# Performance work log

Measured on AMD Instinct MI355X. Metric: run time of the kernel, lower is better.

## Reference

```python
import jax, jax.numpy as jnp
import numpy as np

EMBED_DIM = 128
HIDDEN = 64
LN_EPS = 1e-5
NORM_EPS = 1e-6


def setup_inputs() -> dict:
    key = jax.random.key(0)
    ks = jax.random.split(key, 12)
    B, L = 32, 2048
    inp = {
        "map_lane_positions": jax.random.normal(ks[0], (B, L, 10, 2), dtype=jnp.float32),
        "map_is_intersection": jax.random.randint(ks[1], (B, L), 0, 3, dtype=jnp.int64),
        "map_turn_direction": jax.random.randint(ks[2], (B, L), 0, 3, dtype=jnp.int64),
        "map_traffic_control": jax.random.randint(ks[3], (B, L), 0, 2, dtype=jnp.int64),
        # SingleInputEmbedding params: Linear(2,64) -> LayerNorm(64) -> ReLU -> Linear(64,128)
        "W1": jax.random.normal(ks[4], (2, HIDDEN), dtype=jnp.float32) * 0.5,
        "b1": jax.random.normal(ks[5], (HIDDEN,), dtype=jnp.float32) * 0.1,
        "ln_gamma": jnp.ones((HIDDEN,), dtype=jnp.float32),
        "ln_beta": jnp.zeros((HIDDEN,), dtype=jnp.float32),
        "W2": jax.random.normal(ks[6], (HIDDEN, EMBED_DIM), dtype=jnp.float32) * 0.1,
        "b2": jax.random.normal(ks[7], (EMBED_DIM,), dtype=jnp.float32) * 0.1,
        # discrete embedding tables
        "E_intersection": jax.random.normal(ks[8], (3, EMBED_DIM), dtype=jnp.float32),
        "E_turn": jax.random.normal(ks[9], (3, EMBED_DIM), dtype=jnp.float32),
        "E_traffic": jax.random.normal(ks[10], (2, EMBED_DIM), dtype=jnp.float32),
    }
    return inp


def _mlp(x, W1, b1, g, beta, W2, b2):
    h = x @ W1 + b1                                  # [..., 64]
    mu = jnp.mean(h, axis=-1, keepdims=True)
    var = jnp.mean((h - mu) ** 2, axis=-1, keepdims=True)
    h = (h - mu) * jax.lax.rsqrt(var + LN_EPS) * g + beta
    h = jax.nn.relu(h)
    return h @ W2 + b2                               # [..., 128]


def reference(map_lane_positions, map_is_intersection, map_turn_direction,
              map_traffic_control, W1, b1, ln_gamma, ln_beta, W2, b2,
              E_intersection, E_turn, E_traffic):
    # direction vectors between consecutive points: [B, L, 9, 2]
    dv = map_lane_positions[:, :, 1:, :] - map_lane_positions[:, :, :-1, :]
    norms = jnp.sqrt(jnp.sum(dv ** 2, axis=-1, keepdims=True) + NORM_EPS)
    dv = dv / norms

    cont = _mlp(dv, W1, b1, ln_gamma, ln_beta, W2, b2)   # [B, L, 9, 128]
    # discrete embeddings broadcast over the 9-point axis
    disc = (E_intersection[map_is_intersection]
            + E_turn[map_turn_direction]
            + E_traffic[map_traffic_control])             # [B, L, 128]
    fused = cont + disc[:, :, None, :]                    # [B, L, 9, 128]
    return jnp.max(fused, axis=2)                         # [B, L, 128]
```

## Files before the change

kernel.cpp:

```cpp
#include <hip/hip_runtime.h>
#include <hip/hip_bf16.h>

#define NB      16
#define THREADS 256

#define WS_CST4   0
#define WS_QUAD   256
#define WS_DISC   272
#define WS_W2     2576

typedef float f32x4  __attribute__((ext_vector_type(4)));
typedef short bf16x8 __attribute__((ext_vector_type(8)));

static __device__ __forceinline__ unsigned f2bf(float f) {
    __hip_bfloat16 h = __float2bfloat16(f);
    return (unsigned)__builtin_bit_cast(unsigned short, h);
}

__global__ __launch_bounds__(THREADS)
void lane_setup_kernel(const float* __restrict__ W1, const float* __restrict__ b1,
                       const float* __restrict__ gam, const float* __restrict__ bet,
                       const float* __restrict__ W2, const float* __restrict__ b2,
                       const float* __restrict__ Ei, const float* __restrict__ Et,
                       const float* __restrict__ Etc, float* __restrict__ ws)
{
    const int tid = threadIdx.x, lane = tid & 63, wv = tid >> 6;

    if (wv == 0) {
        float wx = W1[lane], wy = W1[64 + lane], bb = b1[lane];
        float sx = wx, sy = wy, sb = bb;
        #pragma unroll
        for (int m = 1; m < 64; m <<= 1) {
            sx += __shfl_xor(sx, m, 64);
            sy += __shfl_xor(sy, m, 64);
            sb += __shfl_xor(sb, m, 64);
        }
        float a = wx - sx * (1.f / 64.f);
        float b = wy - sy * (1.f / 64.f);
        float c = bb - sb * (1.f / 64.f);
        float p0 = a * a, p1 = b * b, p2 = a * b, p3 = a * c, p4 = b * c, p5 = c * c;
        #pragma unroll
        for (int m = 1; m < 64; m <<= 1) {
            p0 += __shfl_xor(p0, m, 64); p1 += __shfl_xor(p1, m, 64);
            p2 += __shfl_xor(p2, m, 64); p3 += __shfl_xor(p3, m, 64);
            p4 += __shfl_xor(p4, m, 64); p5 += __shfl_xor(p5, m, 64);
        }
        float g = gam[lane];
        ((float4*)(ws + WS_CST4))[lane] = make_float4(a * g, b * g, c * g, bet[lane]);
        if (lane == 0) {
            ws[WS_QUAD + 0] = p0 * (1.f / 64.f);
            ws[WS_QUAD + 1] = p1 * (1.f / 64.f);
            ws[WS_QUAD + 2] = p2 * (1.f / 64.f);
            ws[WS_QUAD + 3] = p3 * (1.f / 64.f);
            ws[WS_QUAD + 4] = p4 * (1.f / 64.f);
            ws[WS_QUAD + 5] = p5 * (1.f / 64.f) + 1e-5f;
        }
    }

    {
        uint4* dst = (uint4*)(ws + WS_W2);
        #pragma unroll
        for (int f = wv * 4; f < wv * 4 + 4; ++f) {
            int c = f >> 1, kt = f & 1;
            int col = c * 16 + (lane & 15);
            int k0  = kt * 32 + (lane >> 4) * 8;
            unsigned w[4];
            #pragma unroll
            for (int j = 0; j < 4; ++j) {
                unsigned lo = f2bf(W2[(k0 + 2 * j) * 128 + col]);
                unsigned hi = f2bf(W2[(k0 + 2 * j + 1) * 128 + col]);
                w[j] = (hi << 16) | lo;
            }
            dst[f * 64 + lane] = make_uint4(w[0], w[1], w[2], w[3]);
        }
    }

    for (int i = tid; i < 18 * 128; i += THREADS) {
        int combo = i >> 7, col = i & 127;
        int ai = combo / 6; int r = combo - ai * 6; int bi = r >> 1; int ci = r & 1;
        ws[WS_DISC + i] = b2[col] + Ei[ai * 128 + col] + Et[bi * 128 + col] + Etc[ci * 128 + col];
    }
}

__global__ __launch_bounds__(THREADS)
void lane_node_embed_mfma(const float* __restrict__ pos,
                          const int*   __restrict__ idx_int,
                          const int*   __restrict__ idx_turn,
                          const int*   __restrict__ idx_tc,
                          const float* __restrict__ ws,
                          float* __restrict__ out,
                          int n_nodes)
{
    __shared__ unsigned short H[NB * 9 * 64];
    __shared__ float4 smv[NB * 9];
    __shared__ int    cmb_lds[NB];

    const int tid  = threadIdx.x;
    const int lane = tid & 63;
    const int wv   = __builtin_amdgcn_readfirstlane(tid >> 6);
    const int blockStart = blockIdx.x * NB;

    const float4 cst = ((const float4*)(ws + WS_CST4))[lane];

    const int ct0 = wv * 2;
    const uint4* wfr = (const uint4*)(ws + WS_W2);
    bf16x8 Bfr[2][2];
    #pragma unroll
    for (int c = 0; c < 2; ++c)
        #pragma unroll
        for (int kt = 0; kt < 2; ++kt)
            Bfr[c][kt] = __builtin_bit_cast(bf16x8, wfr[((ct0 + c) * 2 + kt) * 64 + lane]);

    if (tid < NB * 9) {
        int nd = tid / 9, p = tid - nd * 9;
        int gn = blockStart + nd;
        float ax = 0.f, ay = 0.f, is = 0.f;
        if (gn < n_nodes) {
            const float2* pp = (const float2*)pos + (size_t)gn * 10 + p;
            float2 q0 = pp[0], q1 = pp[1];
            float dx = q1.x - q0.x, dy = q1.y - q0.y;
            float inv = rsqrtf(fmaf(dx, dx, fmaf(dy, dy, 1e-6f)));
            dx *= inv; dy *= inv;
            float qA = ws[WS_QUAD + 0], qB = ws[WS_QUAD + 1], qC = ws[WS_QUAD + 2];
            float qD = ws[WS_QUAD + 3], qE = ws[WS_QUAD + 4], qF = ws[WS_QUAD + 5];
            float t   = fmaf(dx * dy, qC, fmaf(dx, qD, dy * qE));
            float var = fmaf(2.f, t, fmaf(dx * dx, qA, fmaf(dy * dy, qB, qF)));
            is = rsqrtf(var);
            ax = dx * is; ay = dy * is;
        }
        smv[tid] = make_float4(ax, ay, is, 0.f);
    }
    if (tid < NB) {
        int gn = blockStart + tid;
        cmb_lds[tid] = (gn < n_nodes)
            ? (idx_int[gn] * 3 + idx_turn[gn]) * 2 + idx_tc[gn] : 0;
    }
    __syncthreads();

    {
        const int klo    = lane & 7;
        const int kchunk = lane >> 3;
        #pragma unroll
        for (int i = 0; i < 4; ++i) {
            int node = wv * 4 + i;
            int s = node & 7;
            int widx = node * 576 + ((kchunk ^ s) << 3) + klo;
            #pragma unroll
            for (int p = 0; p < 9; ++p) {
                float4 t = smv[node * 9 + p];
                float h = fmaf(t.x, cst.x, fmaf(t.y, cst.y, fmaf(t.z, cst.z, cst.w)));
                h = fmaxf(h, 0.f);
                H[widx + p * 64] = (unsigned short)f2bf(h);
            }
        }
    }
    __syncthreads();

    const int g   = lane >> 4;
    const int l15 = lane & 15;
    const int sr  = l15 & 7;
    const int idx0 = l15 * 576 + (((0 + g) ^ sr) << 3);
    const int idx1 = l15 * 576 + (((4 + g) ^ sr) << 3);

    f32x4 mx0 = {-INFINITY, -INFINITY, -INFINITY, -INFINITY};
    f32x4 mx1 = mx0;
    const f32x4 zz = {0.f, 0.f, 0.f, 0.f};
    #pragma unroll
    for (int p = 0; p < 9; ++p) {
        bf16x8 a0 = *(const bf16x8*)&H[idx0 + p * 64];
        bf16x8 a1 = *(const bf16x8*)&H[idx1 + p * 64];
        f32x4 t0 = __builtin_amdgcn_mfma_f32_16x16x32_bf16(a0, Bfr[0][0], zz, 0, 0, 0);
        t0       = __builtin_amdgcn_mfma_f32_16x16x32_bf16(a1, Bfr[0][1], t0, 0, 0, 0);
        f32x4 t1 = __builtin_amdgcn_mfma_f32_16x16x32_bf16(a0, Bfr[1][0], zz, 0, 0, 0);
        t1       = __builtin_amdgcn_mfma_f32_16x16x32_bf16(a1, Bfr[1][1], t1, 0, 0, 0);
        #pragma unroll
        for (int k = 0; k < 4; ++k) {
            mx0[k] = fmaxf(mx0[k], t0[k]);
            mx1[k] = fmaxf(mx1[k], t1[k]);
        }
    }

    #pragma unroll
    for (int c = 0; c < 2; ++c) {
        int col = (ct0 + c) * 16 + l15;
        f32x4 m = (c == 0) ? mx0 : mx1;
        #pragma unroll
        for (int j = 0; j < 4; ++j) {
            int nd = g * 4 + j;
            int gn = blockStart + nd;
            if (gn < n_nodes) {
                float dv = ws[WS_DISC + cmb_lds[nd] * 128 + col];
                out[(size_t)gn * 128 + col] = m[j] + dv;
            }
        }
    }
}

extern "C" void kernel_launch(void* const* d_in, const int* in_sizes, int n_in,
                              void* d_out, int out_size, void* d_ws, size_t ws_size,
                              hipStream_t stream) {
    const float* pos  = (const float*)d_in[0];
    const int*   ii   = (const int*)  d_in[1];
    const int*   it   = (const int*)  d_in[2];
    const int*   itc  = (const int*)  d_in[3];
    const float* W1   = (const float*)d_in[4];
    const float* b1   = (const float*)d_in[5];
    const float* gam  = (const float*)d_in[6];
    const float* bet  = (const float*)d_in[7];
    const float* W2   = (const float*)d_in[8];
    const float* b2   = (const float*)d_in[9];
    const float* Ei   = (const float*)d_in[10];
    const float* Et   = (const float*)d_in[11];
    const float* Etc  = (const float*)d_in[12];
    float* out = (float*)d_out;
    float* ws  = (float*)d_ws;

    int n_nodes = in_sizes[1];
    int blocks  = (n_nodes + NB - 1) / NB;

    hipLaunchKernelGGL(lane_setup_kernel, dim3(1), dim3(THREADS), 0, stream,
                       W1, b1, gam, bet, W2, b2, Ei, Et, Etc, ws);
    hipLaunchKernelGGL(lane_node_embed_mfma, dim3(blocks), dim3(THREADS), 0, stream,
                       pos, ii, it, itc, ws, out, n_nodes);
}
```

Baseline: 34.83 us.

## Process four node tiles per block with double-buffered LDS and prefetched positions

Each block now handles four 16-node tiles in sequence, loading the W2 fragments and LN constants once per block instead of once per 16 nodes. Hidden activations live in a double-buffered LDS array, and the next tile's position loads are issued before the current tile's MFMA phase, so global latency overlaps compute. The small-vector stash is made wave-local with an lgkmcnt wait instead of a block barrier. The inverse std is stored implicitly and recovered with a sqrt. Each lane now packs two bf16 hidden values per LDS write, and discrete-index lookups are spread across lanes with shuffles. The cost is four times fewer blocks, which lowers parallelism, plus a small numeric difference from recomputing the scale.

```diff
diff --git a/kernel.cpp b/kernel.cpp
--- a/kernel.cpp
+++ b/kernel.cpp
@@ -2,6 +2,7 @@
 #include <hip/hip_bf16.h>
 
 #define NB      16
+#define TILES   4
 #define THREADS 256
 
 #define WS_CST4   0
@@ -91,16 +92,20 @@
                           float* __restrict__ out,
                           int n_nodes)
 {
-    __shared__ unsigned short H[NB * 9 * 64];
-    __shared__ float4 smv[NB * 9];
-    __shared__ int    cmb_lds[NB];
+    __shared__ __align__(16) unsigned short H[2][NB * 9 * 64];
+    __shared__ float2 smv[NB * 9];
 
     const int tid  = threadIdx.x;
     const int lane = tid & 63;
     const int wv   = __builtin_amdgcn_readfirstlane(tid >> 6);
-    const int blockStart = blockIdx.x * NB;
-
-    const float4 cst = ((const float4*)(ws + WS_CST4))[lane];
+    const int blockBase = blockIdx.x * (NB * TILES);
+
+    const float qA = ws[WS_QUAD + 0], qB = ws[WS_QUAD + 1], qC = ws[WS_QUAD + 2];
+    const float qD = ws[WS_QUAD + 3], qE = ws[WS_QUAD + 4], qF = ws[WS_QUAD + 5];
+
+    const int kl = lane & 31;
+    const float4 cstA = ((const float4*)(ws + WS_CST4))[2 * kl];
+    const float4 cstB = ((const float4*)(ws + WS_CST4))[2 * kl + 1];
 
     const int ct0 = wv * 2;
     const uint4* wfr = (const uint4*)(ws + WS_W2);
@@ -111,88 +116,109 @@
         for (int kt = 0; kt < 2; ++kt)
             Bfr[c][kt] = __builtin_bit_cast(bf16x8, wfr[((ct0 + c) * 2 + kt) * 64 + lane]);
 
-    if (tid < NB * 9) {
-        int nd = tid / 9, p = tid - nd * 9;
-        int gn = blockStart + nd;
-        float ax = 0.f, ay = 0.f, is = 0.f;
-        if (gn < n_nodes) {
-            const float2* pp = (const float2*)pos + (size_t)gn * 10 + p;
-            float2 q0 = pp[0], q1 = pp[1];
+    const int sn = lane / 9;
+    const int sp = lane - sn * 9;
+    const int sNodeT = wv * 4 + sn;
+    const bool sAct = (lane < 36);
+
+    float2 q0 = make_float2(0.f, 0.f), q1 = q0;
+
+    const int half = lane >> 5;
+    const int kch  = kl >> 2;
+    const int kofs = (2 * kl) & 7;
+
+    const int l15 = lane & 15, g = lane >> 4;
+    const int sr  = l15 & 7;
+    const int i0  = l15 * 576 + ((g ^ sr) << 3);
+    const int i1  = l15 * 576 + (((4 + g) ^ sr) << 3);
+
+    auto issuePos = [&](int t) {
+        if (sAct) {
+            int gn = blockBase + t * NB + sNodeT;
+            if (gn < n_nodes) {
+                const float2* pp = (const float2*)pos + (size_t)gn * 10 + sp;
+                q0 = pp[0]; q1 = pp[1];
+            } else { q0 = make_float2(0.f, 0.f); q1 = q0; }
+        }
+    };
+
+    auto stashA = [&](int buf) {
+        if (sAct) {
             float dx = q1.x - q0.x, dy = q1.y - q0.y;
             float inv = rsqrtf(fmaf(dx, dx, fmaf(dy, dy, 1e-6f)));
             dx *= inv; dy *= inv;
-            float qA = ws[WS_QUAD + 0], qB = ws[WS_QUAD + 1], qC = ws[WS_QUAD + 2];
-            float qD = ws[WS_QUAD + 3], qE = ws[WS_QUAD + 4], qF = ws[WS_QUAD + 5];
-            float t   = fmaf(dx * dy, qC, fmaf(dx, qD, dy * qE));
-            float var = fmaf(2.f, t, fmaf(dx * dx, qA, fmaf(dy * dy, qB, qF)));
-            is = rsqrtf(var);
-            ax = dx * is; ay = dy * is;
-        }
-        smv[tid] = make_float4(ax, ay, is, 0.f);
-    }
-    if (tid < NB) {
-        int gn = blockStart + tid;
-        cmb_lds[tid] = (gn < n_nodes)
-            ? (idx_int[gn] * 3 + idx_turn[gn]) * 2 + idx_tc[gn] : 0;
-    }
-    __syncthreads();
-
-    {
-        const int klo    = lane & 7;
-        const int kchunk = lane >> 3;
-        #pragma unroll
-        for (int i = 0; i < 4; ++i) {
-            int node = wv * 4 + i;
-            int s = node & 7;
-            int widx = node * 576 + ((kchunk ^ s) << 3) + klo;
+            float tt  = fmaf(dx * dy, qC, fmaf(dx, qD, dy * qE));
+            float var = fmaf(2.f, tt, fmaf(dx * dx, qA, fmaf(dy * dy, qB, qF)));
+            float is  = rsqrtf(var);
+            smv[sNodeT * 9 + sp] = make_float2(dx * is, dy * is);
+        }
+        asm volatile("s_waitcnt lgkmcnt(0)" ::: "memory");
+        #pragma unroll
+        for (int i = 0; i < 2; ++i) {
+            int nd = wv * 4 + 2 * i + half;
+            int base = nd * 576 + ((kch ^ (nd & 7)) << 3) + kofs;
             #pragma unroll
             for (int p = 0; p < 9; ++p) {
-                float4 t = smv[node * 9 + p];
-                float h = fmaf(t.x, cst.x, fmaf(t.y, cst.y, fmaf(t.z, cst.z, cst.w)));
-                h = fmaxf(h, 0.f);
-                H[widx + p * 64] = (unsigned short)f2bf(h);
-            }
-        }
-    }
+                float2 v = smv[nd * 9 + p];
+                float is = sqrtf(fmaf(v.x, v.x, v.y * v.y));
+                float a = fmaf(v.x, cstA.x, fmaf(v.y, cstA.y, fmaf(is, cstA.z, cstA.w)));
+                float b = fmaf(v.x, cstB.x, fmaf(v.y, cstB.y, fmaf(is, cstB.z, cstB.w)));
+                a = fmaxf(a, 0.f); b = fmaxf(b, 0.f);
+                unsigned pk = (f2bf(b) << 16) | f2bf(a);
+                *(unsigned*)&H[buf][base + p * 64] = pk;
+            }
+        }
+    };
+
+    auto phaseB = [&](int t, int buf) {
+        int gnb = blockBase + t * NB;
+        int gn15 = gnb + l15;
+        int cmb = 0;
+        if (gn15 < n_nodes)
+            cmb = (idx_int[gn15] * 3 + idx_turn[gn15]) * 2 + idx_tc[gn15];
+
+        f32x4 mx0 = {-INFINITY, -INFINITY, -INFINITY, -INFINITY};
+        f32x4 mx1 = mx0;
+        const f32x4 zz = {0.f, 0.f, 0.f, 0.f};
+        #pragma unroll
+        for (int p = 0; p < 9; ++p) {
+            bf16x8 a0 = *(const bf16x8*)&H[buf][i0 + p * 64];
+            bf16x8 a1 = *(const bf16x8*)&H[buf][i1 + p * 64];
+            f32x4 t0 = __builtin_amdgcn_mfma_f32_16x16x32_bf16(a0, Bfr[0][0], zz, 0, 0, 0);
+            t0       = __builtin_amdgcn_mfma_f32_16x16x32_bf16(a1, Bfr[0][1], t0, 0, 0, 0);
+            f32x4 t1 = __builtin_amdgcn_mfma_f32_16x16x32_bf16(a0, Bfr[1][0], zz, 0, 0, 0);
+            t1       = __builtin_amdgcn_mfma_f32_16x16x32_bf16(a1, Bfr[1][1], t1, 0, 0, 0);
+            #pragma unroll
+            for (int k = 0; k < 4; ++k) {
+                mx0[k] = fmaxf(mx0[k], t0[k]);
+                mx1[k] = fmaxf(mx1[k], t1[k]);
+            }
+        }
+
+        int col0 = ct0 * 16 + l15;
+        #pragma unroll
+        for (int j = 0; j < 4; ++j) {
+            int nd  = g * 4 + j;
+            int gnj = gnb + nd;
+            int cj  = __shfl(cmb, nd, 64);
+            if (gnj < n_nodes) {
+                float dv0 = ws[WS_DISC + cj * 128 + col0];
+                float dv1 = ws[WS_DISC + cj * 128 + col0 + 16];
+                out[(size_t)gnj * 128 + col0]      = mx0[j] + dv0;
+                out[(size_t)gnj * 128 + col0 + 16] = mx1[j] + dv1;
+            }
+        }
+    };
+
+    issuePos(0);
+    stashA(0);
     __syncthreads();
-
-    const int g   = lane >> 4;
-    const int l15 = lane & 15;
-    const int sr  = l15 & 7;
-    const int idx0 = l15 * 576 + (((0 + g) ^ sr) << 3);
-    const int idx1 = l15 * 576 + (((4 + g) ^ sr) << 3);
-
-    f32x4 mx0 = {-INFINITY, -INFINITY, -INFINITY, -INFINITY};
-    f32x4 mx1 = mx0;
-    const f32x4 zz = {0.f, 0.f, 0.f, 0.f};
     #pragma unroll
-    for (int p = 0; p < 9; ++p) {
-        bf16x8 a0 = *(const bf16x8*)&H[idx0 + p * 64];
-        bf16x8 a1 = *(const bf16x8*)&H[idx1 + p * 64];
-        f32x4 t0 = __builtin_amdgcn_mfma_f32_16x16x32_bf16(a0, Bfr[0][0], zz, 0, 0, 0);
-        t0       = __builtin_amdgcn_mfma_f32_16x16x32_bf16(a1, Bfr[0][1], t0, 0, 0, 0);
-        f32x4 t1 = __builtin_amdgcn_mfma_f32_16x16x32_bf16(a0, Bfr[1][0], zz, 0, 0, 0);
-        t1       = __builtin_amdgcn_mfma_f32_16x16x32_bf16(a1, Bfr[1][1], t1, 0, 0, 0);
-        #pragma unroll
-        for (int k = 0; k < 4; ++k) {
-            mx0[k] = fmaxf(mx0[k], t0[k]);
-            mx1[k] = fmaxf(mx1[k], t1[k]);
-        }
-    }
-
-    #pragma unroll
-    for (int c = 0; c < 2; ++c) {
-        int col = (ct0 + c) * 16 + l15;
-        f32x4 m = (c == 0) ? mx0 : mx1;
-        #pragma unroll
-        for (int j = 0; j < 4; ++j) {
-            int nd = g * 4 + j;
-            int gn = blockStart + nd;
-            if (gn < n_nodes) {
-                float dv = ws[WS_DISC + cmb_lds[nd] * 128 + col];
-                out[(size_t)gn * 128 + col] = m[j] + dv;
-            }
-        }
+    for (int t = 0; t < TILES; ++t) {
+        if (t + 1 < TILES) issuePos(t + 1);
+        phaseB(t, t & 1);
+        if (t + 1 < TILES) stashA((t + 1) & 1);
+        __syncthreads();
     }
 }
 
@@ -216,7 +242,7 @@
     float* ws  = (float*)d_ws;
 
     int n_nodes = in_sizes[1];
-    int blocks  = (n_nodes + NB - 1) / NB;
+    int blocks  = (n_nodes + NB * TILES - 1) / (NB * TILES);
 
     hipLaunchKernelGGL(lane_setup_kernel, dim3(1), dim3(THREADS), 0, stream,
                        W1, b1, gam, bet, W2, b2, Ei, Et, Etc, ws);
```

New measurement: 43.92 us. 1.26x slower.

## Give each wave its own 16-node tile and build MFMA operands in registers

Applied to the files above, without the earlier changes.

Each wavefront now owns a full 16-node tile across all 128 output columns, instead of four waves sharing one tile split by columns. Hidden activations are computed directly into bf16 A-fragments in registers, using shuffles to spread per-point direction data, so the shared-memory staging and both block barriers are gone. The cost is many more registers per wave (eight B-fragment pairs, sixteen float4 constants, eight accumulators), more redundant LayerNorm arithmetic per lane, and a sqrt to rebuild the inverse std. Occupancy may drop as a result.

```diff
diff --git a/kernel.cpp b/kernel.cpp
--- a/kernel.cpp
+++ b/kernel.cpp
@@ -91,107 +91,108 @@
                           float* __restrict__ out,
                           int n_nodes)
 {
-    __shared__ unsigned short H[NB * 9 * 64];
-    __shared__ float4 smv[NB * 9];
-    __shared__ int    cmb_lds[NB];
-
     const int tid  = threadIdx.x;
     const int lane = tid & 63;
-    const int wv   = __builtin_amdgcn_readfirstlane(tid >> 6);
-    const int blockStart = blockIdx.x * NB;
-
-    const float4 cst = ((const float4*)(ws + WS_CST4))[lane];
-
-    const int ct0 = wv * 2;
+    const int wv   = tid >> 6;
+    const int tile = blockIdx.x * 4 + wv;
+    const int base = tile * NB;
+
+    const int l15 = lane & 15;
+    const int g   = lane >> 4;
+
+    const float qA = ws[WS_QUAD + 0], qB = ws[WS_QUAD + 1], qC = ws[WS_QUAD + 2];
+    const float qD = ws[WS_QUAD + 3], qE = ws[WS_QUAD + 4], qF = ws[WS_QUAD + 5];
+
+    float4 cst[16];
+    const float4* c4p = (const float4*)(ws + WS_CST4);
+    #pragma unroll
+    for (int j = 0; j < 8; ++j) {
+        cst[j]     = c4p[g * 8 + j];
+        cst[8 + j] = c4p[32 + g * 8 + j];
+    }
+
     const uint4* wfr = (const uint4*)(ws + WS_W2);
-    bf16x8 Bfr[2][2];
-    #pragma unroll
-    for (int c = 0; c < 2; ++c)
+    bf16x8 Bfr[8][2];
+    #pragma unroll
+    for (int c = 0; c < 8; ++c)
         #pragma unroll
         for (int kt = 0; kt < 2; ++kt)
-            Bfr[c][kt] = __builtin_bit_cast(bf16x8, wfr[((ct0 + c) * 2 + kt) * 64 + lane]);
-
-    if (tid < NB * 9) {
-        int nd = tid / 9, p = tid - nd * 9;
-        int gn = blockStart + nd;
-        float ax = 0.f, ay = 0.f, is = 0.f;
-        if (gn < n_nodes) {
+            Bfr[c][kt] = __builtin_bit_cast(bf16x8, wfr[(c * 2 + kt) * 64 + lane]);
+
+    float axs[3], ays[3];
+    #pragma unroll
+    for (int s = 0; s < 3; ++s) {
+        int p = s * 4 + g;
+        float ax = 0.f, ay = 0.f;
+        int gn = base + l15;
+        if (p < 9 && gn < n_nodes) {
             const float2* pp = (const float2*)pos + (size_t)gn * 10 + p;
             float2 q0 = pp[0], q1 = pp[1];
             float dx = q1.x - q0.x, dy = q1.y - q0.y;
             float inv = rsqrtf(fmaf(dx, dx, fmaf(dy, dy, 1e-6f)));
             dx *= inv; dy *= inv;
-            float qA = ws[WS_QUAD + 0], qB = ws[WS_QUAD + 1], qC = ws[WS_QUAD + 2];
-            float qD = ws[WS_QUAD + 3], qE = ws[WS_QUAD + 4], qF = ws[WS_QUAD + 5];
-            float t   = fmaf(dx * dy, qC, fmaf(dx, qD, dy * qE));
-            float var = fmaf(2.f, t, fmaf(dx * dx, qA, fmaf(dy * dy, qB, qF)));
-            is = rsqrtf(var);
-            ax = dx * is; ay = dy * is;
-        }
-        smv[tid] = make_float4(ax, ay, is, 0.f);
-    }
-    if (tid < NB) {
-        int gn = blockStart + tid;
-        cmb_lds[tid] = (gn < n_nodes)
-            ? (idx_int[gn] * 3 + idx_turn[gn]) * 2 + idx_tc[gn] : 0;
-    }
-    __syncthreads();
-
-    {
-        const int klo    = lane & 7;
-        const int kchunk = lane >> 3;
-        #pragma unroll
-        for (int i = 0; i < 4; ++i) {
-            int node = wv * 4 + i;
-            int s = node & 7;
-            int widx = node * 576 + ((kchunk ^ s) << 3) + klo;
+            float tt  = fmaf(dx * dy, qC, fmaf(dx, qD, dy * qE));
+            float var = fmaf(2.f, tt, fmaf(dx * dx, qA, fmaf(dy * dy, qB, qF)));
+            float is0 = rsqrtf(var);
+            ax = dx * is0; ay = dy * is0;
+        }
+        axs[s] = ax; ays[s] = ay;
+    }
+
+    f32x4 mx[8];
+    #pragma unroll
+    for (int c = 0; c < 8; ++c)
+        mx[c] = (f32x4){-INFINITY, -INFINITY, -INFINITY, -INFINITY};
+    const f32x4 zz = {0.f, 0.f, 0.f, 0.f};
+
+    #pragma unroll
+    for (int p = 0; p < 9; ++p) {
+        const int s = p >> 2;
+        const int o = ((p & 3) << 4) | l15;
+        float ax = __shfl(axs[s], o, 64);
+        float ay = __shfl(ays[s], o, 64);
+        float is = sqrtf(fmaf(ax, ax, ay * ay));
+
+        unsigned w0[4], w1[4];
+        #pragma unroll
+        for (int w = 0; w < 4; ++w) {
+            float4 cA = cst[2 * w], cB = cst[2 * w + 1];
+            float a = fmaxf(fmaf(ax, cA.x, fmaf(ay, cA.y, fmaf(is, cA.z, cA.w))), 0.f);
+            float b = fmaxf(fmaf(ax, cB.x, fmaf(ay, cB.y, fmaf(is, cB.z, cB.w))), 0.f);
+            w0[w] = (f2bf(b) << 16) | f2bf(a);
+            float4 cC = cst[8 + 2 * w], cD = cst[8 + 2 * w + 1];
+            a = fmaxf(fmaf(ax, cC.x, fmaf(ay, cC.y, fmaf(is, cC.z, cC.w))), 0.f);
+            b = fmaxf(fmaf(ax, cD.x, fmaf(ay, cD.y, fmaf(is, cD.z, cD.w))), 0.f);
+            w1[w] = (f2bf(b) << 16) | f2bf(a);
+        }
+        bf16x8 a0 = __builtin_bit_cast(bf16x8, make_uint4(w0[0], w0[1], w0[2], w0[3]));
+        bf16x8 a1 = __builtin_bit_cast(bf16x8, make_uint4(w1[0], w1[1], w1[2], w1[3]));
+
+        #pragma unroll
+        for (int c = 0; c < 8; ++c) {
+            f32x4 t = __builtin_amdgcn_mfma_f32_16x16x32_bf16(a0, Bfr[c][0], zz, 0, 0, 0);
+            t       = __builtin_amdgcn_mfma_f32_16x16x32_bf16(a1, Bfr[c][1], t,  0, 0, 0);
             #pragma unroll
-            for (int p = 0; p < 9; ++p) {
-                float4 t = smv[node * 9 + p];
-                float h = fmaf(t.x, cst.x, fmaf(t.y, cst.y, fmaf(t.z, cst.z, cst.w)));
-                h = fmaxf(h, 0.f);
-                H[widx + p * 64] = (unsigned short)f2bf(h);
-            }
-        }
-    }
-    __syncthreads();
-
-    const int g   = lane >> 4;
-    const int l15 = lane & 15;
-    const int sr  = l15 & 7;
-    const int idx0 = l15 * 576 + (((0 + g) ^ sr) << 3);
-    const int idx1 = l15 * 576 + (((4 + g) ^ sr) << 3);
-
-    f32x4 mx0 = {-INFINITY, -INFINITY, -INFINITY, -INFINITY};
-    f32x4 mx1 = mx0;
-    const f32x4 zz = {0.f, 0.f, 0.f, 0.f};
-    #pragma unroll
-    for (int p = 0; p < 9; ++p) {
-        bf16x8 a0 = *(const bf16x8*)&H[idx0 + p * 64];
-        bf16x8 a1 = *(const bf16x8*)&H[idx1 + p * 64];
-        f32x4 t0 = __builtin_amdgcn_mfma_f32_16x16x32_bf16(a0, Bfr[0][0], zz, 0, 0, 0);
-        t0       = __builtin_amdgcn_mfma_f32_16x16x32_bf16(a1, Bfr[0][1], t0, 0, 0, 0);
-        f32x4 t1 = __builtin_amdgcn_mfma_f32_16x16x32_bf16(a0, Bfr[1][0], zz, 0, 0, 0);
-        t1       = __builtin_amdgcn_mfma_f32_16x16x32_bf16(a1, Bfr[1][1], t1, 0, 0, 0);
-        #pragma unroll
-        for (int k = 0; k < 4; ++k) {
-            mx0[k] = fmaxf(mx0[k], t0[k]);
-            mx1[k] = fmaxf(mx1[k], t1[k]);
-        }
-    }
-
-    #pragma unroll
-    for (int c = 0; c < 2; ++c) {
-        int col = (ct0 + c) * 16 + l15;
-        f32x4 m = (c == 0) ? mx0 : mx1;
-        #pragma unroll
-        for (int j = 0; j < 4; ++j) {
-            int nd = g * 4 + j;
-            int gn = blockStart + nd;
-            if (gn < n_nodes) {
-                float dv = ws[WS_DISC + cmb_lds[nd] * 128 + col];
-                out[(size_t)gn * 128 + col] = m[j] + dv;
-            }
+            for (int k = 0; k < 4; ++k) mx[c][k] = fmaxf(mx[c][k], t[k]);
+        }
+    }
+
+    int gn15 = base + l15;
+    int cmb = 0;
+    if (gn15 < n_nodes)
+        cmb = (idx_int[gn15] * 3 + idx_turn[gn15]) * 2 + idx_tc[gn15];
+
+    #pragma unroll
+    for (int jj = 0; jj < 4; ++jj) {
+        int nd  = g * 4 + jj;
+        int cj  = __shfl(cmb, nd, 64);
+        int gnj = base + nd;
+        if (gnj < n_nodes) {
+            const float* dl = ws + WS_DISC + cj * 128 + l15;
+            float* op = out + (size_t)gnj * 128 + l15;
+            #pragma unroll
+            for (int c = 0; c < 8; ++c)
+                op[c * 16] = mx[c][jj] + dl[c * 16];
         }
     }
 }
@@ -216,7 +217,8 @@
     float* ws  = (float*)d_ws;
 
     int n_nodes = in_sizes[1];
-    int blocks  = (n_nodes + NB - 1) / NB;
+    int tiles   = (n_nodes + NB - 1) / NB;
+    int blocks  = (tiles + 3) / 4;
 
     hipLaunchKernelGGL(lane_setup_kernel, dim3(1), dim3(THREADS), 0, stream,
                        W1, b1, gam, bet, W2, b2, Ei, Et, Etc, ws);
```

After: 44.01 us. 1.26x slower.
